# Performance work log

Measured on AMD Instinct MI355X. Metric: run time of the kernel, lower is better.

## Reference

```python
import jax, jax.numpy as jnp
import numpy as np

B = 8       # number of point clouds
N = 4096    # points per cloud (start_point)
M = 1024    # sampled points per cloud (sampled_point_ammount), ratio 0.25
D = 64      # feature dim


def setup_inputs() -> dict:
    key = jax.random.key(0)
    k1, k2 = jax.random.split(key)
    x = jax.random.normal(k1, (B * N, D), dtype=jnp.float32)
    pos = jax.random.uniform(k2, (B * N, 3), dtype=jnp.float32)
    batch = jnp.repeat(jnp.arange(B, dtype=jnp.int32), N)  # sorted batch ids
    return {"x": x, "pos": pos, "batch": batch}


def _fps_single(pos_b, m):
    # Farthest point sampling on one cloud [N,3]; deterministic start at index 0.
    n = pos_b.shape[0]
    big = jnp.asarray(jnp.finfo(pos_b.dtype).max, pos_b.dtype)

    def step(carry, _):
        mind, last = carry
        d = jnp.sum((pos_b - pos_b[last]) ** 2, axis=-1)  # [N]
        mind = jnp.minimum(mind, d)
        nxt = jnp.argmax(mind).astype(jnp.int32)
        return (mind, nxt), nxt

    init = (jnp.full((n,), big, pos_b.dtype), jnp.int32(0))
    _, rest = jax.lax.scan(step, init, None, length=m - 1)
    return jnp.concatenate([jnp.zeros((1,), jnp.int32), rest])  # [M]


def reference(x, pos, batch):
    pos_b = pos.reshape(B, N, 3)
    # --- DownsampleMRG: FPS gather (scale_factor = M/N) ---
    idx = jax.vmap(lambda p: _fps_single(p, M))(pos_b)              # [B, M] local idx
    gidx = (idx + jnp.arange(B, dtype=jnp.int32)[:, None] * N).reshape(-1)
    x_lr = x[gidx]                                                  # [B*M, D]
    pos_lr = pos[gidx]                                              # [B*M, 3]
    # --- UpsampleMRG: lr_x = cat([x_lr, pos_lr]); knn_interpolate k=1 ---
    lr_feat = jnp.concatenate([x_lr, pos_lr], axis=1).reshape(B, M, D + 3)
    pos_lr_b = pos_lr.reshape(B, M, 3)
    # pairwise squared distances hr->lr within each cloud: [B, N, M]
    d2 = jnp.sum((pos_b[:, :, None, :] - pos_lr_b[:, None, :, :]) ** 2, axis=-1)
    nn = jnp.argmin(d2, axis=-1)                                    # [B, N]
    # k=1 interpolation: weights normalize to 1 -> pure nearest-neighbor gather
    interp = jnp.take_along_axis(lr_feat, nn[:, :, None], axis=1).reshape(B * N, D + 3)
    # out_x = cat([x_hr, pos_hr, interpolated lr features])
    out_x = jnp.concatenate([x, pos, interp], axis=1)               # [B*N, D+3+D+3]
    return out_x, jnp.zeros((out_x.shape[0], 3), pos.dtype), batch
```

## Files before the change

### kernel.cpp

```cpp
#include <hip/hip_runtime.h>
#include <cstdint>

#define BATCH 8
#define NPTS  4096
#define MPTS  1024
#define DIM   64

typedef float v2f __attribute__((ext_vector_type(2)));
typedef unsigned long long u64;
typedef unsigned int u32;

__device__ __forceinline__ double mk_key(float m, u32 aux) {
  return __hiloint2double((int)__float_as_uint(m), (int)aux);
}
__device__ __forceinline__ u32 key_lo(double d) {
  return (u32)__double2loint(d);
}

#define WAVE_MAX_F64_STEP(x, ctrl)                                                   \
  {                                                                                  \
    const int lo_ = __builtin_amdgcn_update_dpp(0, __double2loint(x), (ctrl), 0xf, 0xf, true); \
    const int hi_ = __builtin_amdgcn_update_dpp(0, __double2hiint(x), (ctrl), 0xf, 0xf, true); \
    const double y_ = __hiloint2double(hi_, lo_);                                    \
    (x) = fmax((x), y_);                                                             \
  }

__global__ __launch_bounds__(512) void fps_kernel(const float* __restrict__ pos,
                                                  int* __restrict__ gidx) {
#pragma clang fp contract(off)
  const int b = blockIdx.x;
  const int t = threadIdx.x;
  const float* p = pos + (size_t)b * NPTS * 3;

  __shared__ float sx[NPTS], sy[NPTS], sz[NPTS];
  __shared__ double red[2][8];

  v2f px[4], py[4], pz[4], mind[4];
  u32 aux[8];
#pragma unroll
  for (int k = 0; k < 8; ++k) {
    const int i = t + k * 512;
    aux[k] = ~(u32)i;
    const float a = p[3 * i + 0];
    const float c = p[3 * i + 1];
    const float d = p[3 * i + 2];
    sx[i] = a; sy[i] = c; sz[i] = d;
    px[k >> 1][k & 1] = a;
    py[k >> 1][k & 1] = c;
    pz[k >> 1][k & 1] = d;
    mind[k >> 1][k & 1] = 3.402823466e+38f;
  }
  __syncthreads();

  if (t == 0) gidx[b * MPTS] = b * NPTS;
  float lx = sx[0], ly = sy[0], lz = sz[0];

  for (int it = 1; it < MPTS; ++it) {
    const v2f vlx = {lx, lx}, vly = {ly, ly}, vlz = {lz, lz};
    double pg[4];
#pragma unroll
    for (int g = 0; g < 4; ++g) {
      const v2f dx = px[g] - vlx;
      const v2f dy = py[g] - vly;
      const v2f dz = pz[g] - vlz;
      const v2f d = (dx * dx + dy * dy) + dz * dz;
      const v2f m = __builtin_elementwise_min(mind[g], d);
      mind[g] = m;
      pg[g] = fmax(mk_key(m[0], aux[2 * g]), mk_key(m[1], aux[2 * g + 1]));
    }
    double best = fmax(fmax(pg[0], pg[1]), fmax(pg[2], pg[3]));

    WAVE_MAX_F64_STEP(best, 0x111);
    WAVE_MAX_F64_STEP(best, 0x112);
    WAVE_MAX_F64_STEP(best, 0x114);
    WAVE_MAX_F64_STEP(best, 0x118);
    WAVE_MAX_F64_STEP(best, 0x142);
    WAVE_MAX_F64_STEP(best, 0x143);

    const int buf = it & 1;
    if ((t & 63) == 63) red[buf][t >> 6] = best;
    __syncthreads();

    const double c0 = fmax(fmax(red[buf][0], red[buf][1]),
                           fmax(red[buf][2], red[buf][3]));
    const double c1 = fmax(fmax(red[buf][4], red[buf][5]),
                           fmax(red[buf][6], red[buf][7]));
    const double c = fmax(c0, c1);
    const u32 widx = ~key_lo(c);

    lx = sx[widx];
    ly = sy[widx];
    lz = sz[widx];
    if (t == 0) gidx[b * MPTS + it] = b * NPTS + (int)widx;
  }
}

__global__ __launch_bounds__(256) void nn_assemble_kernel(
    const float* __restrict__ x, const float* __restrict__ pos,
    const int* __restrict__ gidx, float* __restrict__ out) {
#pragma clang fp contract(off)
  const int b = blockIdx.x >> 5;
  const int chunk = blockIdx.x & 31;
  const int t = threadIdx.x;

  __shared__ float lrx[MPTS], lry[MPTS], lrz[MPTS];
  __shared__ int snng[128];
  for (int j = t; j < MPTS; j += 256) {
    const int g = gidx[b * MPTS + j];
    lrx[j] = pos[3 * g + 0];
    lry[j] = pos[3 * g + 1];
    lrz[j] = pos[3 * g + 2];
  }
  __syncthreads();

  {
    const int pt = chunk * 128 + (t >> 1);
    const int half = t & 1;
    const int i = b * NPTS + pt;
    const float px = pos[3 * i + 0];
    const float py = pos[3 * i + 1];
    const float pz = pos[3 * i + 2];
    const v2f vx = {px, px}, vy = {py, py}, vz = {pz, pz};

    double best = __hiloint2double(0x7FEFFFFF, 0xFFFFFFFF);
    const int j0 = half * 512;
#pragma unroll 4
    for (int s = 0; s < 256; ++s) {
      const int j = j0 + 2 * s;
      const v2f qx = *(const v2f*)&lrx[j];
      const v2f qy = *(const v2f*)&lry[j];
      const v2f qz = *(const v2f*)&lrz[j];
      const v2f dx = vx - qx;
      const v2f dy = vy - qy;
      const v2f dz = vz - qz;
      const v2f d = (dx * dx + dy * dy) + dz * dz;
      best = fmin(best, fmin(mk_key(d[0], (u32)j), mk_key(d[1], (u32)(j + 1))));
    }
    const int blo = __shfl_xor(__double2loint(best), 1, 64);
    const int bhi = __shfl_xor(__double2hiint(best), 1, 64);
    best = fmin(best, __hiloint2double(bhi, blo));
    if (half == 0) snng[t >> 1] = gidx[b * MPTS + (int)key_lo(best)];
  }
  __syncthreads();

  const int wave = t >> 6, lane = t & 63;
  float* o2 = out + (size_t)BATCH * NPTS * 134;
  float* o3 = o2 + (size_t)BATCH * NPTS * 3;
#pragma unroll
  for (int r = wave; r < 128; r += 4) {
    const int i = b * NPTS + chunk * 128 + r;
    const int g = snng[r];
    float* o = out + (size_t)i * 134;
    o[lane] = x[(size_t)i * DIM + lane];
    o[67 + lane] = x[(size_t)g * DIM + lane];
    if (lane < 3) {
      o[64 + lane] = pos[3 * i + lane];
      o[131 + lane] = pos[3 * g + lane];
      o2[3 * i + lane] = 0.0f;
    }
    if (lane == 0) o3[i] = (float)b;
  }
}

extern "C" void kernel_launch(void* const* d_in, const int* in_sizes, int n_in,
                              void* d_out, int out_size, void* d_ws, size_t ws_size,
                              hipStream_t stream) {
  const float* x = (const float*)d_in[0];
  const float* pos = (const float*)d_in[1];

  int* gidx = (int*)d_ws;
  float* out = (float*)d_out;

  fps_kernel<<<BATCH, 512, 0, stream>>>(pos, gidx);
  nn_assemble_kernel<<<BATCH * 32, 256, 0, stream>>>(x, pos, gidx, out);
}
```

Baseline: 637.2 us.

## Halve FPS block size, fold min-distance into packed keys, use float4 LDS

The FPS kernel drops from 512 to 256 threads per block, so each thread holds 16 points and the cross-wave reduction handles 4 partial maxima instead of 8. The running min-distance and the index now live in one 64-bit key, updated with an f64 fmin. Point coordinates are stored as float4 in shared memory so the winner is fetched with one load. Packed f32 add/mul are forced through inline asm in both kernels, and the NN search loads float4 from LDS. The aim is shorter barrier and reduction cost per FPS iteration, paid for with more serial work and register pressure per thread.

```diff
diff --git a/kernel.cpp b/kernel.cpp
--- a/kernel.cpp
+++ b/kernel.cpp
@@ -10,12 +10,17 @@
 typedef unsigned long long u64;
 typedef unsigned int u32;
 
-__device__ __forceinline__ double mk_key(float m, u32 aux) {
-  return __hiloint2double((int)__float_as_uint(m), (int)aux);
+__device__ __forceinline__ v2f pk_add(v2f a, v2f b) {
+  v2f d; asm("v_pk_add_f32 %0, %1, %2" : "=v"(d) : "v"(a), "v"(b)); return d;
 }
-__device__ __forceinline__ u32 key_lo(double d) {
-  return (u32)__double2loint(d);
+__device__ __forceinline__ v2f pk_mul(v2f a, v2f b) {
+  v2f d; asm("v_pk_mul_f32 %0, %1, %2" : "=v"(d) : "v"(a), "v"(b)); return d;
 }
+
+__device__ __forceinline__ double mk_key_bits(int dist_bits, int lo) {
+  return __hiloint2double(dist_bits, lo);
+}
+__device__ __forceinline__ u32 key_lo(double d) { return (u32)__double2loint(d); }
 
 #define WAVE_MAX_F64_STEP(x, ctrl)                                                   \
   {                                                                                  \
@@ -25,50 +30,63 @@
     (x) = fmax((x), y_);                                                             \
   }
 
-__global__ __launch_bounds__(512) void fps_kernel(const float* __restrict__ pos,
+__global__ __launch_bounds__(256) void fps_kernel(const float* __restrict__ pos,
                                                   int* __restrict__ gidx) {
 #pragma clang fp contract(off)
   const int b = blockIdx.x;
   const int t = threadIdx.x;
   const float* p = pos + (size_t)b * NPTS * 3;
 
-  __shared__ float sx[NPTS], sy[NPTS], sz[NPTS];
-  __shared__ double red[2][8];
+  __shared__ float4 sp[NPTS];
+  __shared__ double red[2][4];
 
-  v2f px[4], py[4], pz[4], mind[4];
-  u32 aux[8];
+  v2f px[8], py[8], pz[8];
+  double state[16];
 #pragma unroll
-  for (int k = 0; k < 8; ++k) {
-    const int i = t + k * 512;
-    aux[k] = ~(u32)i;
+  for (int k = 0; k < 16; ++k) {
+    const int i = t + k * 256;
     const float a = p[3 * i + 0];
     const float c = p[3 * i + 1];
     const float d = p[3 * i + 2];
-    sx[i] = a; sy[i] = c; sz[i] = d;
+    sp[i] = make_float4(a, c, d, 0.0f);
     px[k >> 1][k & 1] = a;
     py[k >> 1][k & 1] = c;
     pz[k >> 1][k & 1] = d;
-    mind[k >> 1][k & 1] = 3.402823466e+38f;
+    state[k] = mk_key_bits(0x7F7FFFFF, (int)~(u32)i);
   }
   __syncthreads();
 
   if (t == 0) gidx[b * MPTS] = b * NPTS;
-  float lx = sx[0], ly = sy[0], lz = sz[0];
+  float4 w = sp[0];
+  float lx = w.x, ly = w.y, lz = w.z;
 
   for (int it = 1; it < MPTS; ++it) {
-    const v2f vlx = {lx, lx}, vly = {ly, ly}, vlz = {lz, lz};
-    double pg[4];
+    const v2f vnx = {-lx, -lx}, vny = {-ly, -ly}, vnz = {-lz, -lz};
 #pragma unroll
-    for (int g = 0; g < 4; ++g) {
-      const v2f dx = px[g] - vlx;
-      const v2f dy = py[g] - vly;
-      const v2f dz = pz[g] - vlz;
-      const v2f d = (dx * dx + dy * dy) + dz * dz;
-      const v2f m = __builtin_elementwise_min(mind[g], d);
-      mind[g] = m;
-      pg[g] = fmax(mk_key(m[0], aux[2 * g]), mk_key(m[1], aux[2 * g + 1]));
+    for (int g = 0; g < 8; ++g) {
+      const v2f dx = pk_add(px[g], vnx);
+      const v2f dy = pk_add(py[g], vny);
+      const v2f dz = pk_add(pz[g], vnz);
+      const v2f xx = pk_mul(dx, dx);
+      const v2f yy = pk_mul(dy, dy);
+      const v2f zz = pk_mul(dz, dz);
+      const v2f s  = pk_add(xx, yy);
+      const v2f d  = pk_add(s, zz);
+      const double c0 = mk_key_bits(__float_as_int(d[0]), __double2loint(state[2 * g]));
+      const double c1 = mk_key_bits(__float_as_int(d[1]), __double2loint(state[2 * g + 1]));
+      state[2 * g]     = fmin(state[2 * g], c0);
+      state[2 * g + 1] = fmin(state[2 * g + 1], c1);
     }
-    double best = fmax(fmax(pg[0], pg[1]), fmax(pg[2], pg[3]));
+    double m0 = fmax(state[0], state[1]);
+    double m1 = fmax(state[2], state[3]);
+    double m2 = fmax(state[4], state[5]);
+    double m3 = fmax(state[6], state[7]);
+    double m4 = fmax(state[8], state[9]);
+    double m5 = fmax(state[10], state[11]);
+    double m6 = fmax(state[12], state[13]);
+    double m7 = fmax(state[14], state[15]);
+    double best = fmax(fmax(fmax(m0, m1), fmax(m2, m3)),
+                       fmax(fmax(m4, m5), fmax(m6, m7)));
 
     WAVE_MAX_F64_STEP(best, 0x111);
     WAVE_MAX_F64_STEP(best, 0x112);
@@ -81,16 +99,12 @@
     if ((t & 63) == 63) red[buf][t >> 6] = best;
     __syncthreads();
 
-    const double c0 = fmax(fmax(red[buf][0], red[buf][1]),
-                           fmax(red[buf][2], red[buf][3]));
-    const double c1 = fmax(fmax(red[buf][4], red[buf][5]),
-                           fmax(red[buf][6], red[buf][7]));
-    const double c = fmax(c0, c1);
+    const double c = fmax(fmax(red[buf][0], red[buf][1]),
+                          fmax(red[buf][2], red[buf][3]));
     const u32 widx = ~key_lo(c);
 
-    lx = sx[widx];
-    ly = sy[widx];
-    lz = sz[widx];
+    w = sp[widx];
+    lx = w.x; ly = w.y; lz = w.z;
     if (t == 0) gidx[b * MPTS + it] = b * NPTS + (int)widx;
   }
 }
@@ -103,7 +117,7 @@
   const int chunk = blockIdx.x & 31;
   const int t = threadIdx.x;
 
-  __shared__ float lrx[MPTS], lry[MPTS], lrz[MPTS];
+  __shared__ __align__(16) float lrx[MPTS], lry[MPTS], lrz[MPTS];
   __shared__ int snng[128];
   for (int j = t; j < MPTS; j += 256) {
     const int g = gidx[b * MPTS + j];
@@ -117,24 +131,32 @@
     const int pt = chunk * 128 + (t >> 1);
     const int half = t & 1;
     const int i = b * NPTS + pt;
-    const float px = pos[3 * i + 0];
-    const float py = pos[3 * i + 1];
-    const float pz = pos[3 * i + 2];
-    const v2f vx = {px, px}, vy = {py, py}, vz = {pz, pz};
+    const float qx = pos[3 * i + 0];
+    const float qy = pos[3 * i + 1];
+    const float qz = pos[3 * i + 2];
+    const v2f vnx = {-qx, -qx}, vny = {-qy, -qy}, vnz = {-qz, -qz};
 
     double best = __hiloint2double(0x7FEFFFFF, 0xFFFFFFFF);
     const int j0 = half * 512;
 #pragma unroll 4
-    for (int s = 0; s < 256; ++s) {
-      const int j = j0 + 2 * s;
-      const v2f qx = *(const v2f*)&lrx[j];
-      const v2f qy = *(const v2f*)&lry[j];
-      const v2f qz = *(const v2f*)&lrz[j];
-      const v2f dx = vx - qx;
-      const v2f dy = vy - qy;
-      const v2f dz = vz - qz;
-      const v2f d = (dx * dx + dy * dy) + dz * dz;
-      best = fmin(best, fmin(mk_key(d[0], (u32)j), mk_key(d[1], (u32)(j + 1))));
+    for (int s = 0; s < 128; ++s) {
+      const int j = j0 + 4 * s;
+      const float4 qxv = *(const float4*)&lrx[j];
+      const float4 qyv = *(const float4*)&lry[j];
+      const float4 qzv = *(const float4*)&lrz[j];
+      const v2f x01 = {qxv.x, qxv.y}, x23 = {qxv.z, qxv.w};
+      const v2f y01 = {qyv.x, qyv.y}, y23 = {qyv.z, qyv.w};
+      const v2f z01 = {qzv.x, qzv.y}, z23 = {qzv.z, qzv.w};
+      const v2f dx0 = pk_add(x01, vnx), dx1 = pk_add(x23, vnx);
+      const v2f dy0 = pk_add(y01, vny), dy1 = pk_add(y23, vny);
+      const v2f dz0 = pk_add(z01, vnz), dz1 = pk_add(z23, vnz);
+      const v2f d0 = pk_add(pk_add(pk_mul(dx0, dx0), pk_mul(dy0, dy0)), pk_mul(dz0, dz0));
+      const v2f d1 = pk_add(pk_add(pk_mul(dx1, dx1), pk_mul(dy1, dy1)), pk_mul(dz1, dz1));
+      const double c0 = mk_key_bits(__float_as_int(d0[0]), j + 0);
+      const double c1 = mk_key_bits(__float_as_int(d0[1]), j + 1);
+      const double c2 = mk_key_bits(__float_as_int(d1[0]), j + 2);
+      const double c3 = mk_key_bits(__float_as_int(d1[1]), j + 3);
+      best = fmin(best, fmin(fmin(c0, c1), fmin(c2, c3)));
     }
     const int blo = __shfl_xor(__double2loint(best), 1, 64);
     const int bhi = __shfl_xor(__double2hiint(best), 1, 64);
@@ -171,6 +193,6 @@
   int* gidx = (int*)d_ws;
   float* out = (float*)d_out;
 
-  fps_kernel<<<BATCH, 512, 0, stream>>>(pos, gidx);
+  fps_kernel<<<BATCH, 256, 0, stream>>>(pos, gidx);
   nn_assemble_kernel<<<BATCH * 32, 256, 0, stream>>>(x, pos, gidx, out);
 }
```

Result: no change. 648.8 us (+1.8%).
